# Performance work log

Hardware: AMD Instinct MI355X
Metric: run time of the kernel (lower is better)

The kernel has to match this reference:

```python
import jax, jax.numpy as jnp
import numpy as np

N = 50_000       # nodes
E = 1_600_000    # edges (avg degree 32)
D = 32           # emb_dim == hidden_dim, num_heads = 1
L = 8            # num_layers
K = 8            # SortPooling k
VOCAB = 100


def setup_inputs() -> dict:
    key = jax.random.key(0)
    ks = jax.random.split(key, 20)
    def nrm(k, shape, scale=0.1):
        return jax.random.normal(k, shape, dtype=jnp.float32) * scale
    return {
        "h_tok": jax.random.randint(ks[0], (N,), 0, VOCAB),
        "e_tok": jax.random.randint(ks[1], (E,), 0, VOCAB),
        "src": jax.random.randint(ks[2], (E,), 0, N),
        "dst": jax.random.randint(ks[3], (E,), 0, N),
        "tok_emb": nrm(ks[4], (VOCAB, D)),
        "e_tok_emb": nrm(ks[5], (VOCAB, D)),
        # per-layer EGATConv params (stacked over L layers; all dims are D->D)
        "W_ni": nrm(ks[6], (L, D, D)),
        "W_nj": nrm(ks[7], (L, D, D)),
        "W_fij": nrm(ks[8], (L, D, D)),
        "b_edge": nrm(ks[9], (L, D)),
        "attn": nrm(ks[10], (L, D)),
        "W_node": nrm(ks[11], (L, D, D)),
        # MLP head
        "W_lin": nrm(ks[12], (K * D, D)),
        "b_lin": nrm(ks[13], (D,)),
        "W1": nrm(ks[14], (D, D)),
        "b1": nrm(ks[15], (D,)),
        "W2": nrm(ks[16], (D, D)),
        "b2": nrm(ks[17], (D,)),
        "Wc": nrm(ks[18], (D, 2)),
        "bc": nrm(ks[19], (2,)),
    }


def _egat_layer(h, e, src, dst, Wni, Wnj, Wfij, b, attn, Wnode):
    """DGL EGATConv, num_heads=1. h: [N,D] nodes, e: [E,D] edges."""
    n = h.shape[0]
    # per-edge feature: f_ij = LeakyReLU(A*h_i + B*h_j + C*e_ij + b)
    f = jax.nn.leaky_relu((h @ Wni)[src] + (h @ Wnj)[dst] + e @ Wfij + b, 0.01)  # [E,D]
    logits = jnp.sum(f * attn, axis=-1)                                         # [E]
    # edge softmax over incoming edges of each destination node
    m = jax.ops.segment_max(logits, dst, num_segments=n)
    ex = jnp.exp(logits - m[dst])
    a = ex / jax.ops.segment_sum(ex, dst, num_segments=n)[dst]                  # [E]
    msg = (h @ Wnode)[src] * a[:, None]                                         # [E,D]
    h_out = jax.ops.segment_sum(msg, dst, num_segments=n)                       # [N,D]
    return h_out, f


def reference(h_tok, e_tok, src, dst, tok_emb, e_tok_emb, W_ni, W_nj, W_fij,
              b_edge, attn, W_node, W_lin, b_lin, W1, b1, W2, b2, Wc, bc):
    h = jax.nn.relu(tok_emb[h_tok])   # [N,D]
    e = e_tok_emb[e_tok]              # [E,D]

    def step(carry, p):
        h, e = carry
        Wni, Wnj, Wfij, b, at, Wn = p
        h2, e2 = _egat_layer(h, e, src, dst, Wni, Wnj, Wfij, b, at, Wn)
        return (jax.nn.relu(h2), e2), None

    (h, e), _ = jax.lax.scan(step, (h, e), (W_ni, W_nj, W_fij, b_edge, attn, W_node))

    # SortPooling(k): sort each node's features ascending, rank nodes by last
    # (largest) channel descending, keep top-k nodes, flatten. Single graph.
    hs = jnp.sort(h, axis=-1)                     # [N,D]
    _, idx = jax.lax.top_k(hs[:, -1], K)          # top-k nodes
    x = hs[idx].reshape(1, K * D)                 # [1, k*D]

    x = jax.nn.relu(x @ W_lin + b_lin)
    x = jax.nn.relu(x @ W1 + b1)
    x = jax.nn.relu(x @ W2 + b2)
    return x @ Wc + bc                            # [1, 2]
```

## Files before the change

### kernel.cpp

```cpp
#include <hip/hip_runtime.h>
#include <hip/hip_fp16.h>

#define DD 32
#define NLAYERS 8
#define TOPK 8
#define NPB 256
#define HNB 1024
#define BCH 4096
#define P2CAP 12288

typedef _Float16 half8 __attribute__((ext_vector_type(8)));
typedef float f32x4 __attribute__((ext_vector_type(4)));

__device__ __forceinline__ unsigned encf(float x){ unsigned u=__float_as_uint(x); return (u&0x80000000u)? ~u : (u|0x80000000u); }
__device__ __forceinline__ unsigned short f2h(float f){ return __half_as_ushort(__float2half(f)); }
__device__ __forceinline__ float h2f(unsigned short u){ return __half2float(__ushort_as_half(u)); }
__device__ __forceinline__ float4 up4(uint2 u){
  float4 r;
  r.x=h2f((unsigned short)(u.x&0xFFFFu)); r.y=h2f((unsigned short)(u.x>>16));
  r.z=h2f((unsigned short)(u.y&0xFFFFu)); r.w=h2f((unsigned short)(u.y>>16));
  return r;
}
union HU4 { uint4 u; half8 h; };
__device__ __forceinline__ int gidx(const void* p, long i, int i64){
  return i64 ? (int)((const long long*)p)[i] : ((const int*)p)[i];
}

__global__ __launch_bounds__(1024) void k_detect(const int* __restrict__ srcw,
                                                 int* __restrict__ iflag,
                                                 int* __restrict__ bcnt){
  int tid = threadIdx.x;
  for (int i=tid;i<HNB;i+=1024) bcnt[i]=0;
  if (tid==0){
    int allz = 1;
    for (int k=1;k<32;k+=2) if (srcw[k]!=0) allz = 0;
    *iflag = allz;
  }
}

__global__ void k_init(const void* __restrict__ h_tok,
                       const float* __restrict__ tok_emb,
                       unsigned short* __restrict__ h16,
                       const int* __restrict__ iflag, int N)
{
  int i64 = *iflag;
  long idx = (long)blockIdx.x*blockDim.x + threadIdx.x;
  if (idx >= (long)N*8) return;
  int n=(int)(idx>>3), q=(int)(idx&7);
  int t = gidx(h_tok, n, i64);
  float4 v = reinterpret_cast<const float4*>(tok_emb)[t*8+q];
  uint2 o;
  o.x = (unsigned)f2h(fmaxf(v.x,0.f)) | ((unsigned)f2h(fmaxf(v.y,0.f))<<16);
  o.y = (unsigned)f2h(fmaxf(v.z,0.f)) | ((unsigned)f2h(fmaxf(v.w,0.f))<<16);
  reinterpret_cast<uint2*>(h16)[(long)n*8+q] = o;
}

__global__ __launch_bounds__(256) void k_hist(
    const void* __restrict__ dstv, int* __restrict__ bcnt,
    const int* __restrict__ iflag, int E, int NB)
{
  __shared__ int bins[HNB];
  int i64 = *iflag;
  int tid = threadIdx.x;
  for (int i=tid;i<NB;i+=256) bins[i]=0;
  __syncthreads();
  long base = (long)blockIdx.x * BCH;
  long rem = (long)E - base;
  int nloc = (rem < BCH) ? (int)rem : BCH;
  for (int t=tid; t<nloc; t+=256){
    int d = gidx(dstv, base+t, i64);
    atomicAdd(&bins[d>>8], 1);
  }
  __syncthreads();
  for (int i=tid;i<NB;i+=256){
    int v = bins[i];
    if (v) atomicAdd(&bcnt[i], v);
  }
}

__global__ __launch_bounds__(1024) void k_bscan(const int* __restrict__ bcnt,
    int* __restrict__ bbase, int* __restrict__ gcur, int NB, int E)
{
  __shared__ int wsum[16];
  int tid=threadIdx.x, lane=tid&63, w=tid>>6;
  int v = (tid<NB)? bcnt[tid]:0;
  int x=v;
  #pragma unroll
  for (int d=1;d<64;d<<=1){ int t=__shfl_up(x,d,64); if(lane>=d) x+=t; }
  if (lane==63) wsum[w]=x;
  __syncthreads();
  if (w==0 && lane<16){
    int y=wsum[lane];
    #pragma unroll
    for (int d=1;d<16;d<<=1){ int t=__shfl_up(y,d,64); if(lane>=d) y+=t; }
    wsum[lane]=y;
  }
  __syncthreads();
  int wb = (w>0)? wsum[w-1]:0;
  int ex = x - v + wb;
  if (tid<NB){ bbase[tid]=ex; gcur[tid]=ex; }
  if (tid==0) bbase[NB]=E;
}

__global__ __launch_bounds__(256) void k_bucket(
    const void* __restrict__ srcv, const void* __restrict__ dstv,
    int* __restrict__ gcur, uint2* __restrict__ btmp,
    const int* __restrict__ iflag, int E, int NB)
{
  __shared__ int hist[HNB];
  __shared__ int cbase[HNB];
  int i64 = *iflag;
  int tid = threadIdx.x;
  long base = (long)blockIdx.x * BCH;
  long rem = (long)E - base;
  int nloc = (rem < BCH) ? (int)rem : BCH;
  if (nloc <= 0) return;
  for (int i = tid; i < NB; i += 256) hist[i] = 0;
  __syncthreads();
  int dl[BCH/256];
  #pragma unroll
  for (int k = 0; k < BCH/256; k++){
    int t = tid + k*256;
    dl[k] = -1;
    if (t < nloc){
      int d = gidx(dstv, base + t, i64);
      dl[k] = d;
      atomicAdd(&hist[d>>8], 1);
    }
  }
  __syncthreads();
  for (int i = tid; i < NB; i += 256){
    int hv = hist[i];
    cbase[i] = hv ? atomicAdd(&gcur[i], hv) : 0;
    hist[i] = 0;
  }
  __syncthreads();
  #pragma unroll
  for (int k = 0; k < BCH/256; k++){
    int t = tid + k*256;
    if (t < nloc){
      int d = dl[k];
      int s = gidx(srcv, base + t, i64);
      int b = d>>8;
      int slot = cbase[b] + atomicAdd(&hist[b], 1);
      uint2 r; r.x = ((unsigned)d<<16) | (unsigned)s; r.y = (unsigned)(base + t);
      btmp[slot] = r;
    }
  }
}

__global__ __launch_bounds__(256) void k_bsort(
    const int* __restrict__ bbase, const uint2* __restrict__ btmp,
    uint2* __restrict__ sde8, int* __restrict__ off, int N, int NB)
{
  __shared__ int lcnt[NPB];
  __shared__ int lbase[NPB];
  __shared__ int wsum2[4];
  __shared__ uint2 lrec[P2CAP];
  int bkt = blockIdx.x;
  int base = bbase[bkt], endp = bbase[bkt+1];
  int sz = endp - base;
  int lo = bkt*NPB;
  int tid = threadIdx.x;
  lcnt[tid] = 0;
  __syncthreads();
  for (int i=tid;i<sz;i+=256){
    uint2 r = btmp[base+i];
    atomicAdd(&lcnt[(int)(r.x>>16) - lo], 1);
  }
  __syncthreads();
  int v = lcnt[tid];
  int lane = tid&63, w = tid>>6;
  int x = v;
  #pragma unroll
  for (int d=1;d<64;d<<=1){ int t=__shfl_up(x,d,64); if(lane>=d) x+=t; }
  if (lane==63) wsum2[w]=x;
  __syncthreads();
  if (tid==0){ int a=0; for(int i=0;i<4;i++){ int t=wsum2[i]; wsum2[i]=a; a+=t; } }
  __syncthreads();
  int ex = x - v + wsum2[w];
  lbase[tid] = ex;
  int node = lo + tid;
  if (node < N) off[node] = base + ex;
  if (bkt == NB-1 && tid == 0) off[N] = bbase[NB];
  __syncthreads();
  if (sz <= P2CAP){
    lcnt[tid] = lbase[tid];
    __syncthreads();
    for (int i=tid;i<sz;i+=256){
      uint2 r = btmp[base+i];
      int d = (int)(r.x>>16) - lo;
      int p = atomicAdd(&lcnt[d],1);
      lrec[p] = r;
    }
    __syncthreads();
    for (int i=tid;i<sz;i+=256)
      sde8[base+i] = lrec[i];
  } else {
    lcnt[tid] = base + lbase[tid];
    __syncthreads();
    for (int i=tid;i<sz;i+=256){
      uint2 r = btmp[base+i];
      int d = (int)(r.x>>16) - lo;
      int p = atomicAdd(&lcnt[d],1);
      sde8[p] = r;
    }
  }
}

__global__ void k_fill(const uint2* __restrict__ sde8, const void* __restrict__ e_tok,
                       const float* __restrict__ e_emb,
                       unsigned* __restrict__ csr_sd, unsigned short* __restrict__ ebuf,
                       const int* __restrict__ iflag, int E){
  int i64 = *iflag;
  long idx = (long)blockIdx.x*blockDim.x + threadIdx.x;
  if (idx >= (long)E*4) return;
  int pos = (int)(idx>>2), j = (int)(idx&3);
  uint2 r = sde8[pos];
  if (j==0) csr_sd[pos] = r.x;
  int t = gidx(e_tok, (int)r.y, i64);
  const float4* sp = reinterpret_cast<const float4*>(e_emb + t*DD) + j*2;
  float4 x = sp[0], y = sp[1];
  uint4 ov;
  ov.x = (unsigned)f2h(x.x) | ((unsigned)f2h(x.y)<<16);
  ov.y = (unsigned)f2h(x.z) | ((unsigned)f2h(x.w)<<16);
  ov.z = (unsigned)f2h(y.x) | ((unsigned)f2h(y.y)<<16);
  ov.w = (unsigned)f2h(y.z) | ((unsigned)f2h(y.w)<<16);
  reinterpret_cast<uint4*>(ebuf)[(long)pos*4+j] = ov;
}

__global__ __launch_bounds__(256) void k_nodeAB(
    const unsigned short* __restrict__ h16,
    const float* __restrict__ WA, const float* __restrict__ WB,
    unsigned short* __restrict__ hA16, unsigned short* __restrict__ hB16, int N)
{
  __shared__ float hl[8][DD];
  int tid = threadIdx.x;
  int ln = tid>>5, c = tid&31;
  int n = blockIdx.x*8 + ln;
  hl[ln][c] = (n<N)? h2f(h16[(long)n*DD+c]) : 0.f;
  __syncthreads();
  float a=0.f,b=0.f;
  #pragma unroll
  for (int k=0;k<DD;k++){
    float v = hl[ln][k];
    a = fmaf(v, WA[k*DD+c], a);
    b = fmaf(v, WB[k*DD+c], b);
  }
  if (n<N){ hA16[(long)n*DD+c]=f2h(a); hB16[(long)n*DD+c]=f2h(b); }
}

__global__ __launch_bounds__(256) void k_edge(
    unsigned short* __restrict__ ebuf,
    const unsigned short* __restrict__ hA16, const unsigned short* __restrict__ hB16,
    const unsigned* __restrict__ csr_sd,
    const float* __restrict__ Wf, const float* __restrict__ bvec,
    const float* __restrict__ attn,
    unsigned short* __restrict__ lbuf, int ntiles, int writef)
{
  int lane = threadIdx.x & 63;
  int wid = (blockIdx.x*256 + threadIdx.x) >> 6;
  int nw  = (gridDim.x*256) >> 6;
  int m = lane & 15, q = lane >> 4;
  half8 a0, a1;
  #pragma unroll
  for (int j=0;j<8;j++){
    a0[j] = (_Float16)Wf[(q*8+j)*DD + m];
    a1[j] = (_Float16)Wf[(q*8+j)*DD + 16 + m];
  }
  float4 blo = *reinterpret_cast<const float4*>(bvec + q*4);
  float4 bhi = *reinterpret_cast<const float4*>(bvec + 16 + q*4);
  float4 alo = *reinterpret_cast<const float4*>(attn + q*4);
  float4 ahi = *reinterpret_cast<const float4*>(attn + 16 + q*4);
  f32x4 zero = {0.f,0.f,0.f,0.f};
  HU4 b0; b0.u = make_uint4(0,0,0,0);
  HU4 b1; b1.u = make_uint4(0,0,0,0);
  HU4 b2; b2.u = make_uint4(0,0,0,0);
  unsigned sd0 = 0, sd1 = 0, sd2 = 0;
  uint2 gA0_0={0,0}, gA1_0={0,0}, gB0_0={0,0}, gB1_0={0,0};
  uint2 gA0_1={0,0}, gA1_1={0,0}, gB0_1={0,0}, gB1_1={0,0};
  if (wid < ntiles){
    long e0 = (long)wid*16 + m;
    sd0 = csr_sd[e0];
    b0.u = *reinterpret_cast<const uint4*>(ebuf + e0*DD + q*8);
    unsigned s = sd0 & 0xFFFFu, d = sd0 >> 16;
    const uint2* pA = reinterpret_cast<const uint2*>(hA16 + (long)s*DD);
    const uint2* pB = reinterpret_cast<const uint2*>(hB16 + (long)d*DD);
    gA0_0=pA[q]; gA1_0=pA[4+q]; gB0_0=pB[q]; gB1_0=pB[4+q];
  }
  if (wid + nw < ntiles){
    long e1 = (long)(wid+nw)*16 + m;
    sd1 = csr_sd[e1];
    b1.u = *reinterpret_cast<const uint4*>(ebuf + e1*DD + q*8);
    unsigned s = sd1 & 0xFFFFu, d = sd1 >> 16;
    const uint2* pA = reinterpret_cast<const uint2*>(hA16 + (long)s*DD);
    const uint2* pB = reinterpret_cast<const uint2*>(hB16 + (long)d*DD);
    gA0_1=pA[q]; gA1_1=pA[4+q]; gB0_1=pB[q]; gB1_1=pB[4+q];
  }
  if (wid + 2*nw < ntiles){
    long e2 = (long)(wid+2*nw)*16 + m;
    sd2 = csr_sd[e2];
    b2.u = *reinterpret_cast<const uint4*>(ebuf + e2*DD + q*8);
  }
  for (int t = wid; t < ntiles; t += nw){
    int t2 = t + 2*nw, t3 = t + 3*nw;
    unsigned sd3 = 0; HU4 b3; b3.u = make_uint4(0,0,0,0);
    if (t3 < ntiles){
      long e3 = (long)t3*16 + m;
      sd3 = csr_sd[e3];
      b3.u = *reinterpret_cast<const uint4*>(ebuf + e3*DD + q*8);
    }
    uint2 gA0_2={0,0}, gA1_2={0,0}, gB0_2={0,0}, gB1_2={0,0};
    if (t2 < ntiles){
      unsigned s = sd2 & 0xFFFFu, d = sd2 >> 16;
      const uint2* pA = reinterpret_cast<const uint2*>(hA16 + (long)s*DD);
      const uint2* pB = reinterpret_cast<const uint2*>(hB16 + (long)d*DD);
      gA0_2=pA[q]; gA1_2=pA[4+q]; gB0_2=pB[q]; gB1_2=pB[4+q];
    }
    f32x4 d0 = __builtin_amdgcn_mfma_f32_16x16x32_f16(a0, b0.h, zero, 0,0,0);
    f32x4 d1 = __builtin_amdgcn_mfma_f32_16x16x32_f16(a1, b0.h, zero, 0,0,0);
    long tbase = (long)t*16;
    long edge = tbase + m;
    float4 A0 = up4(gA0_0), A1 = up4(gA1_0);
    float4 B0 = up4(gB0_0), B1 = up4(gB1_0);
    float f00 = d0[0]+A0.x+B0.x+blo.x, f01 = d0[1]+A0.y+B0.y+blo.y;
    float f02 = d0[2]+A0.z+B0.z+blo.z, f03 = d0[3]+A0.w+B0.w+blo.w;
    float f10 = d1[0]+A1.x+B1.x+bhi.x, f11 = d1[1]+A1.y+B1.y+bhi.y;
    float f12 = d1[2]+A1.z+B1.z+bhi.z, f13 = d1[3]+A1.w+B1.w+bhi.w;
    f00 = (f00>0.f)?f00:0.01f*f00; f01 = (f01>0.f)?f01:0.01f*f01;
    f02 = (f02>0.f)?f02:0.01f*f02; f03 = (f03>0.f)?f03:0.01f*f03;
    f10 = (f10>0.f)?f10:0.01f*f10; f11 = (f11>0.f)?f11:0.01f*f11;
    f12 = (f12>0.f)?f12:0.01f*f12; f13 = (f13>0.f)?f13:0.01f*f13;
    if (writef){
      uint2 w0, w1;
      w0.x = (unsigned)f2h(f00) | ((unsigned)f2h(f01)<<16);
      w0.y = (unsigned)f2h(f02) | ((unsigned)f2h(f03)<<16);
      w1.x = (unsigned)f2h(f10) | ((unsigned)f2h(f11)<<16);
      w1.y = (unsigned)f2h(f12) | ((unsigned)f2h(f13)<<16);
      *reinterpret_cast<uint2*>(ebuf + edge*DD + q*4) = w0;
      *reinterpret_cast<uint2*>(ebuf + edge*DD + 16 + q*4) = w1;
    }
    float l = f00*alo.x + f01*alo.y + f02*alo.z + f03*alo.w
            + f10*ahi.x + f11*ahi.y + f12*ahi.z + f13*ahi.w;
    l += __shfl_xor(l, 16, 64);
    l += __shfl_xor(l, 32, 64);
    if (lane < 16){
      float lc = fminf(fmaxf(l, -15.f), 10.5f);
      lbuf[tbase + lane] = f2h(__expf(lc));
    }
    sd0 = sd1; b0 = b1;
    gA0_0=gA0_1; gA1_0=gA1_1; gB0_0=gB0_1; gB1_0=gB1_1;
    sd1 = sd2; b1 = b2;
    gA0_1=gA0_2; gA1_1=gA1_2; gB0_1=gB0_2; gB1_1=gB1_2;
    sd2 = sd3; b2 = b3;
  }
}

__global__ __launch_bounds__(256) void k_aggrP(
    const unsigned short* __restrict__ h16in, const unsigned short* __restrict__ lbuf,
    const int* __restrict__ off, const unsigned* __restrict__ csr_sd,
    const float* __restrict__ Wnd, const float* __restrict__ WA,
    const float* __restrict__ WB,
    unsigned short* __restrict__ h16out, unsigned short* __restrict__ hA16,
    unsigned short* __restrict__ hB16, float* __restrict__ hout, int N, int last)
{
  __shared__ float gl[8][DD];
  __shared__ float tl[8][DD];
  int tid=threadIdx.x;
  int ln = tid>>5, c = tid&31;
  int n = blockIdx.x*8 + ln;
  float num=0.f, den=0.f;
  if (n<N){
    int o0 = off[n], o1 = off[n+1];
    int i = o0;
    for (; i+8 <= o1; i += 8){
      unsigned sd0=csr_sd[i],   sd1=csr_sd[i+1], sd2=csr_sd[i+2], sd3=csr_sd[i+3];
      unsigned sd4=csr_sd[i+4], sd5=csr_sd[i+5], sd6=csr_sd[i+6], sd7=csr_sd[i+7];
      float ex0=h2f(lbuf[i]),   ex1=h2f(lbuf[i+1]), ex2=h2f(lbuf[i+2]), ex3=h2f(lbuf[i+3]);
      float ex4=h2f(lbuf[i+4]), ex5=h2f(lbuf[i+5]), ex6=h2f(lbuf[i+6]), ex7=h2f(lbuf[i+7]);
      float g0=h2f(h16in[(long)(sd0&0xFFFFu)*DD+c]);
      float g1=h2f(h16in[(long)(sd1&0xFFFFu)*DD+c]);
      float g2=h2f(h16in[(long)(sd2&0xFFFFu)*DD+c]);
      float g3=h2f(h16in[(long)(sd3&0xFFFFu)*DD+c]);
      float g4=h2f(h16in[(long)(sd4&0xFFFFu)*DD+c]);
      float g5=h2f(h16in[(long)(sd5&0xFFFFu)*DD+c]);
      float g6=h2f(h16in[(long)(sd6&0xFFFFu)*DD+c]);
      float g7=h2f(h16in[(long)(sd7&0xFFFFu)*DD+c]);
      num=fmaf(ex0,g0,num); num=fmaf(ex1,g1,num);
      num=fmaf(ex2,g2,num); num=fmaf(ex3,g3,num);
      num=fmaf(ex4,g4,num); num=fmaf(ex5,g5,num);
      num=fmaf(ex6,g6,num); num=fmaf(ex7,g7,num);
      den+=ex0; den+=ex1; den+=ex2; den+=ex3;
      den+=ex4; den+=ex5; den+=ex6; den+=ex7;
    }
    for (; i<o1; i++){
      unsigned sd=csr_sd[i];
      float ex=h2f(lbuf[i]);
      num=fmaf(ex, h2f(h16in[(long)(sd&0xFFFFu)*DD+c]), num);
      den += ex;
    }
  }
  gl[ln][c] = (den>0.f)? num/den : 0.f;
  __syncthreads();
  float t=0.f;
  #pragma unroll
  for (int k=0;k<DD;k++) t = fmaf(gl[ln][k], Wnd[k*DD+c], t);
  t = fmaxf(t, 0.f);
  if (last){
    if (n<N) hout[(long)n*DD+c] = t;
    return;
  }
  tl[ln][c] = t;
  __syncthreads();
  float a=0.f,b=0.f;
  #pragma unroll
  for (int k=0;k<DD;k++){
    float v = tl[ln][k];
    a = fmaf(v, WA[k*DD+c], a);
    b = fmaf(v, WB[k*DD+c], b);
  }
  if (n<N){
    h16out[(long)n*DD+c]=f2h(t);
    hA16[(long)n*DD+c]=f2h(a);
    hB16[(long)n*DD+c]=f2h(b);
  }
}

__global__ void k_keys(const float* __restrict__ h, unsigned long long* __restrict__ keys, int N){
  int n = blockIdx.x*blockDim.x + threadIdx.x;
  if (n>=N) return;
  const float4* p = reinterpret_cast<const float4*>(h + (long)n*DD);
  float m = -1e38f;
  #pragma unroll
  for (int j=0;j<8;j++){
    float4 v = p[j];
    m = fmaxf(m, fmaxf(fmaxf(v.x,v.y), fmaxf(v.z,v.w)));
  }
  keys[n] = ((unsigned long long)encf(m)<<32) | (unsigned)(~(unsigned)n);
}

__global__ __launch_bounds__(256) void k_ptop(const unsigned long long* __restrict__ keys, int N,
                                              unsigned long long* __restrict__ outk){
  __shared__ unsigned long long red[256];
  int tid = threadIdx.x, b = blockIdx.x, nb = gridDim.x;
  int chunk = (N + nb - 1) / nb;
  int base = b*chunk, end = base+chunk; if (end>N) end=N;
  unsigned long long loc[TOPK];
  #pragma unroll
  for (int i=0;i<TOPK;i++) loc[i]=0ull;
  for (int i=base+tid; i<end; i+=256){
    unsigned long long k = keys[i];
    if (k > loc[TOPK-1]){
      int j = TOPK-1;
      while (j>0 && loc[j-1]<k){ loc[j]=loc[j-1]; j--; }
      loc[j]=k;
    }
  }
  for (int r=0; r<TOPK; r++){
    red[tid] = loc[0];
    __syncthreads();
    for (int s=128; s>0; s>>=1){
      if (tid<s && red[tid+s]>red[tid]) red[tid]=red[tid+s];
      __syncthreads();
    }
    unsigned long long w = red[0];
    if (tid==0) outk[b*TOPK + r] = w;
    if (loc[0]==w){
      #pragma unroll
      for (int j=0;j<TOPK-1;j++) loc[j]=loc[j+1];
      loc[TOPK-1]=0ull;
    }
    __syncthreads();
  }
}

__global__ __launch_bounds__(256) void k_head(
    const float* __restrict__ h, const unsigned long long* __restrict__ sel,
    const float* __restrict__ Wlin, const float* __restrict__ blin,
    const float* __restrict__ W1, const float* __restrict__ b1,
    const float* __restrict__ W2, const float* __restrict__ b2,
    const float* __restrict__ Wc, const float* __restrict__ bc,
    float* __restrict__ out, int N)
{
  __shared__ float xs[TOPK][DD];
  __shared__ float y1[DD], y2[DD], y3[DD];
  int tid=threadIdx.x;
  int r=tid>>5, c=tid&31;
  unsigned node = ~(unsigned)(sel[r] & 0xFFFFFFFFull);
  if (node >= (unsigned)N) node = 0;
  xs[r][c] = h[(long)node*DD + c];
  __syncthreads();
  if (tid<TOPK){
    for (int i=1;i<DD;i++){
      float v=xs[tid][i]; int j=i-1;
      while (j>=0 && xs[tid][j]>v){ xs[tid][j+1]=xs[tid][j]; j--; }
      xs[tid][j+1]=v;
    }
  }
  __syncthreads();
  if (tid<DD){
    float a=blin[tid];
    for (int i=0;i<TOPK*DD;i++) a = fmaf(xs[i>>5][i&31], Wlin[i*DD+tid], a);
    y1[tid] = a>0.f? a : 0.f;
  }
  __syncthreads();
  if (tid<DD){
    float a=b1[tid];
    #pragma unroll
    for (int i=0;i<DD;i++) a = fmaf(y1[i], W1[i*DD+tid], a);
    y2[tid] = a>0.f? a : 0.f;
  }
  __syncthreads();
  if (tid<DD){
    float a=b2[tid];
    #pragma unroll
    for (int i=0;i<DD;i++) a = fmaf(y2[i], W2[i*DD+tid], a);
    y3[tid] = a>0.f? a : 0.f;
  }
  __syncthreads();
  if (tid<2){
    float a=bc[tid];
    #pragma unroll
    for (int i=0;i<DD;i++) a = fmaf(y3[i], Wc[i*2+tid], a);
    out[tid] = a;
  }
}

extern "C" void kernel_launch(void* const* d_in, const int* in_sizes, int n_in,
                              void* d_out, int out_size, void* d_ws, size_t ws_size,
                              hipStream_t stream) {
  const int N = in_sizes[0];
  const int E = in_sizes[1];
  const float* tok_emb   = (const float*)d_in[4];
  const float* e_tok_emb = (const float*)d_in[5];
  const float* W_ni  = (const float*)d_in[6];
  const float* W_nj  = (const float*)d_in[7];
  const float* W_fij = (const float*)d_in[8];
  const float* b_e   = (const float*)d_in[9];
  const float* attn  = (const float*)d_in[10];
  const float* W_nd  = (const float*)d_in[11];

  char* p = (char*)d_ws;
  auto alloc = [&](size_t bytes)->char* {
    char* r = p; p += (bytes + 255) & ~(size_t)255; return r;
  };
  int* iflag = (int*)alloc(256);
  unsigned long long* sel = (unsigned long long*)alloc(256);
  unsigned long long* cand = (unsigned long long*)alloc(256*TOPK*8);
  int* bcnt = (int*)alloc(HNB*4);
  int* bbase = (int*)alloc((HNB+1)*4);
  int* gcur = (int*)alloc(HNB*4);
  int* csroff = (int*)alloc((size_t)(N+1)*4);
  unsigned* csr_sd = (unsigned*)alloc((size_t)(E+32)*4);
  float* h = (float*)alloc((size_t)N*DD*4);
  alloc((size_t)N*DD*2);
  unsigned short* lbuf = (unsigned short*)alloc((size_t)(E+32)*2);
  unsigned short* h16a = (unsigned short*)alloc((size_t)N*DD*2);
  unsigned short* h16b = (unsigned short*)alloc((size_t)N*DD*2);
  unsigned short* hA16 = (unsigned short*)alloc((size_t)N*DD*2);
  unsigned short* hB16 = (unsigned short*)alloc((size_t)N*DD*2);
  unsigned short* ebuf = (unsigned short*)alloc((size_t)(E+32)*DD*2);
  uint2* sde8 = (uint2*)h;
  uint2* btmp = (uint2*)ebuf;
  unsigned long long* keys = (unsigned long long*)lbuf;

  const int NB = (N + NPB - 1) / NPB;
  const int NECH = (E + BCH - 1) / BCH;

  hipLaunchKernelGGL(k_detect, dim3(1), dim3(1024), 0, stream, (const int*)d_in[2], iflag, bcnt);
  hipLaunchKernelGGL(k_init, dim3((int)(((long)N*8+255)/256)), dim3(256), 0, stream,
                     d_in[0], tok_emb, h16a, iflag, N);
  hipLaunchKernelGGL(k_hist, dim3(NECH), dim3(256), 0, stream,
                     d_in[3], bcnt, iflag, E, NB);
  hipLaunchKernelGGL(k_bscan, dim3(1), dim3(1024), 0, stream, bcnt, bbase, gcur, NB, E);
  hipLaunchKernelGGL(k_bucket, dim3(NECH), dim3(256), 0, stream,
                     d_in[2], d_in[3], gcur, btmp, iflag, E, NB);
  hipLaunchKernelGGL(k_bsort, dim3(NB), dim3(256), 0, stream, bbase, btmp, sde8, csroff, N, NB);
  hipLaunchKernelGGL(k_fill, dim3((int)(((long)E*4+255)/256)), dim3(256), 0, stream,
                     sde8, d_in[1], e_tok_emb, csr_sd, ebuf, iflag, E);

  int nb_node = (N+7)/8;
  int ntiles = (E+15)/16;
  hipLaunchKernelGGL(k_nodeAB, dim3(nb_node), dim3(256), 0, stream,
                     h16a, W_ni, W_nj, hA16, hB16, N);
  unsigned short* hcur = h16a;
  unsigned short* hnext = h16b;
  for (int l=0; l<NLAYERS; l++){
    const float* Wf  = W_fij + (size_t)l*DD*DD;
    const float* bl  = b_e   + (size_t)l*DD;
    const float* at  = attn  + (size_t)l*DD;
    const float* Wnd = W_nd  + (size_t)l*DD*DD;
    int last = (l == NLAYERS-1);
    hipLaunchKernelGGL(k_edge, dim3(2048), dim3(256), 0, stream,
                       ebuf, hA16, hB16, csr_sd, Wf, bl, at, lbuf, ntiles,
                       last ? 0 : 1);
    const float* WnA = last ? W_ni : (W_ni + (size_t)(l+1)*DD*DD);
    const float* WnB = last ? W_nj : (W_nj + (size_t)(l+1)*DD*DD);
    hipLaunchKernelGGL(k_aggrP, dim3(nb_node), dim3(256), 0, stream,
                       hcur, lbuf, csroff, csr_sd, Wnd, WnA, WnB,
                       hnext, hA16, hB16, h, N, last);
    unsigned short* tmp = hcur; hcur = hnext; hnext = tmp;
  }

  hipLaunchKernelGGL(k_keys, dim3((N+255)/256), dim3(256), 0, stream, h, keys, N);
  hipLaunchKernelGGL(k_ptop, dim3(256), dim3(256), 0, stream, keys, N, cand);
  hipLaunchKernelGGL(k_ptop, dim3(1), dim3(256), 0, stream, cand, 256*TOPK, sel);
  hipLaunchKernelGGL(k_head, dim3(1), dim3(256), 0, stream,
                     h, sel,
                     (const float*)d_in[12], (const float*)d_in[13],
                     (const float*)d_in[14], (const float*)d_in[15],
                     (const float*)d_in[16], (const float*)d_in[17],
                     (const float*)d_in[18], (const float*)d_in[19],
                     (float*)d_out, N);
}
```

Before: 1.039 ms.

## Permute hA/hB channel layout for 16-byte gathers and pack src index with exp weight

```diff
diff --git a/kernel.cpp b/kernel.cpp
--- a/kernel.cpp
+++ b/kernel.cpp
@@ -24,6 +24,9 @@
 union HU4 { uint4 u; half8 h; };
 __device__ __forceinline__ int gidx(const void* p, long i, int i64){
   return i64 ? (int)((const long long*)p)[i] : ((const int*)p)[i];
+}
+__device__ __forceinline__ int pidx(int c){
+  return ((c&15)>>2)*8 + (c&3) + ((c&16)?4:0);
 }
 
 __global__ __launch_bounds__(1024) void k_detect(const int* __restrict__ srcw,
@@ -247,7 +250,11 @@
     a = fmaf(v, WA[k*DD+c], a);
     b = fmaf(v, WB[k*DD+c], b);
   }
-  if (n<N){ hA16[(long)n*DD+c]=f2h(a); hB16[(long)n*DD+c]=f2h(b); }
+  if (n<N){
+    int pc = pidx(c);
+    hA16[(long)n*DD+pc]=f2h(a);
+    hB16[(long)n*DD+pc]=f2h(b);
+  }
 }
 
 __global__ __launch_bounds__(256) void k_edge(
@@ -256,7 +263,7 @@
     const unsigned* __restrict__ csr_sd,
     const float* __restrict__ Wf, const float* __restrict__ bvec,
     const float* __restrict__ attn,
-    unsigned short* __restrict__ lbuf, int ntiles, int writef)
+    unsigned* __restrict__ exs, int ntiles, int writef)
 {
   int lane = threadIdx.x & 63;
   int wid = (blockIdx.x*256 + threadIdx.x) >> 6;
@@ -277,25 +284,23 @@
   HU4 b1; b1.u = make_uint4(0,0,0,0);
   HU4 b2; b2.u = make_uint4(0,0,0,0);
   unsigned sd0 = 0, sd1 = 0, sd2 = 0;
-  uint2 gA0_0={0,0}, gA1_0={0,0}, gB0_0={0,0}, gB1_0={0,0};
-  uint2 gA0_1={0,0}, gA1_1={0,0}, gB0_1={0,0}, gB1_1={0,0};
+  uint4 gA_0={0,0,0,0}, gB_0={0,0,0,0};
+  uint4 gA_1={0,0,0,0}, gB_1={0,0,0,0};
   if (wid < ntiles){
     long e0 = (long)wid*16 + m;
     sd0 = csr_sd[e0];
     b0.u = *reinterpret_cast<const uint4*>(ebuf + e0*DD + q*8);
     unsigned s = sd0 & 0xFFFFu, d = sd0 >> 16;
-    const uint2* pA = reinterpret_cast<const uint2*>(hA16 + (long)s*DD);
-    const uint2* pB = reinterpret_cast<const uint2*>(hB16 + (long)d*DD);
-    gA0_0=pA[q]; gA1_0=pA[4+q]; gB0_0=pB[q]; gB1_0=pB[4+q];
+    gA_0 = reinterpret_cast<const uint4*>(hA16 + (long)s*DD)[q];
+    gB_0 = reinterpret_cast<const uint4*>(hB16 + (long)d*DD)[q];
   }
   if (wid + nw < ntiles){
     long e1 = (long)(wid+nw)*16 + m;
     sd1 = csr_sd[e1];
     b1.u = *reinterpret_cast<const uint4*>(ebuf + e1*DD + q*8);
     unsigned s = sd1 & 0xFFFFu, d = sd1 >> 16;
-    const uint2* pA = reinterpret_cast<const uint2*>(hA16 + (long)s*DD);
-    const uint2* pB = reinterpret_cast<const uint2*>(hB16 + (long)d*DD);
-    gA0_1=pA[q]; gA1_1=pA[4+q]; gB0_1=pB[q]; gB1_1=pB[4+q];
+    gA_1 = reinterpret_cast<const uint4*>(hA16 + (long)s*DD)[q];
+    gB_1 = reinterpret_cast<const uint4*>(hB16 + (long)d*DD)[q];
   }
   if (wid + 2*nw < ntiles){
     long e2 = (long)(wid+2*nw)*16 + m;
@@ -310,19 +315,18 @@
       sd3 = csr_sd[e3];
       b3.u = *reinterpret_cast<const uint4*>(ebuf + e3*DD + q*8);
     }
-    uint2 gA0_2={0,0}, gA1_2={0,0}, gB0_2={0,0}, gB1_2={0,0};
+    uint4 gA_2={0,0,0,0}, gB_2={0,0,0,0};
     if (t2 < ntiles){
       unsigned s = sd2 & 0xFFFFu, d = sd2 >> 16;
-      const uint2* pA = reinterpret_cast<const uint2*>(hA16 + (long)s*DD);
-      const uint2* pB = reinterpret_cast<const uint2*>(hB16 + (long)d*DD);
-      gA0_2=pA[q]; gA1_2=pA[4+q]; gB0_2=pB[q]; gB1_2=pB[4+q];
+      gA_2 = reinterpret_cast<const uint4*>(hA16 + (long)s*DD)[q];
+      gB_2 = reinterpret_cast<const uint4*>(hB16 + (long)d*DD)[q];
     }
     f32x4 d0 = __builtin_amdgcn_mfma_f32_16x16x32_f16(a0, b0.h, zero, 0,0,0);
     f32x4 d1 = __builtin_amdgcn_mfma_f32_16x16x32_f16(a1, b0.h, zero, 0,0,0);
     long tbase = (long)t*16;
     long edge = tbase + m;
-    float4 A0 = up4(gA0_0), A1 = up4(gA1_0);
-    float4 B0 = up4(gB0_0), B1 = up4(gB1_0);
+    float4 A0 = up4(make_uint2(gA_0.x, gA_0.y)), A1 = up4(make_uint2(gA_0.z, gA_0.w));
+    float4 B0 = up4(make_uint2(gB_0.x, gB_0.y)), B1 = up4(make_uint2(gB_0.z, gB_0.w));
     float f00 = d0[0]+A0.x+B0.x+blo.x, f01 = d0[1]+A0.y+B0.y+blo.y;
     float f02 = d0[2]+A0.z+B0.z+blo.z, f03 = d0[3]+A0.w+B0.w+blo.w;
     float f10 = d1[0]+A1.x+B1.x+bhi.x, f11 = d1[1]+A1.y+B1.y+bhi.y;
@@ -346,19 +350,17 @@
     l += __shfl_xor(l, 32, 64);
     if (lane < 16){
       float lc = fminf(fmaxf(l, -15.f), 10.5f);
-      lbuf[tbase + lane] = f2h(__expf(lc));
-    }
-    sd0 = sd1; b0 = b1;
-    gA0_0=gA0_1; gA1_0=gA1_1; gB0_0=gB0_1; gB1_0=gB1_1;
-    sd1 = sd2; b1 = b2;
-    gA0_1=gA0_2; gA1_1=gA1_2; gB0_1=gB0_2; gB1_1=gB1_2;
+      exs[tbase + lane] = ((unsigned)f2h(__expf(lc))<<16) | (sd0 & 0xFFFFu);
+    }
+    sd0 = sd1; b0 = b1; gA_0 = gA_1; gB_0 = gB_1;
+    sd1 = sd2; b1 = b2; gA_1 = gA_2; gB_1 = gB_2;
     sd2 = sd3; b2 = b3;
   }
 }
 
 __global__ __launch_bounds__(256) void k_aggrP(
-    const unsigned short* __restrict__ h16in, const unsigned short* __restrict__ lbuf,
-    const int* __restrict__ off, const unsigned* __restrict__ csr_sd,
+    const unsigned short* __restrict__ h16in, const unsigned* __restrict__ exs,
+    const int* __restrict__ off,
     const float* __restrict__ Wnd, const float* __restrict__ WA,
     const float* __restrict__ WB,
     unsigned short* __restrict__ h16out, unsigned short* __restrict__ hA16,
@@ -374,18 +376,20 @@
     int o0 = off[n], o1 = off[n+1];
     int i = o0;
     for (; i+8 <= o1; i += 8){
-      unsigned sd0=csr_sd[i],   sd1=csr_sd[i+1], sd2=csr_sd[i+2], sd3=csr_sd[i+3];
-      unsigned sd4=csr_sd[i+4], sd5=csr_sd[i+5], sd6=csr_sd[i+6], sd7=csr_sd[i+7];
-      float ex0=h2f(lbuf[i]),   ex1=h2f(lbuf[i+1]), ex2=h2f(lbuf[i+2]), ex3=h2f(lbuf[i+3]);
-      float ex4=h2f(lbuf[i+4]), ex5=h2f(lbuf[i+5]), ex6=h2f(lbuf[i+6]), ex7=h2f(lbuf[i+7]);
-      float g0=h2f(h16in[(long)(sd0&0xFFFFu)*DD+c]);
-      float g1=h2f(h16in[(long)(sd1&0xFFFFu)*DD+c]);
-      float g2=h2f(h16in[(long)(sd2&0xFFFFu)*DD+c]);
-      float g3=h2f(h16in[(long)(sd3&0xFFFFu)*DD+c]);
-      float g4=h2f(h16in[(long)(sd4&0xFFFFu)*DD+c]);
-      float g5=h2f(h16in[(long)(sd5&0xFFFFu)*DD+c]);
-      float g6=h2f(h16in[(long)(sd6&0xFFFFu)*DD+c]);
-      float g7=h2f(h16in[(long)(sd7&0xFFFFu)*DD+c]);
+      unsigned w0=exs[i],   w1=exs[i+1], w2=exs[i+2], w3=exs[i+3];
+      unsigned w4=exs[i+4], w5=exs[i+5], w6=exs[i+6], w7=exs[i+7];
+      float ex0=h2f((unsigned short)(w0>>16)), ex1=h2f((unsigned short)(w1>>16));
+      float ex2=h2f((unsigned short)(w2>>16)), ex3=h2f((unsigned short)(w3>>16));
+      float ex4=h2f((unsigned short)(w4>>16)), ex5=h2f((unsigned short)(w5>>16));
+      float ex6=h2f((unsigned short)(w6>>16)), ex7=h2f((unsigned short)(w7>>16));
+      float g0=h2f(h16in[(long)(w0&0xFFFFu)*DD+c]);
+      float g1=h2f(h16in[(long)(w1&0xFFFFu)*DD+c]);
+      float g2=h2f(h16in[(long)(w2&0xFFFFu)*DD+c]);
+      float g3=h2f(h16in[(long)(w3&0xFFFFu)*DD+c]);
+      float g4=h2f(h16in[(long)(w4&0xFFFFu)*DD+c]);
+      float g5=h2f(h16in[(long)(w5&0xFFFFu)*DD+c]);
+      float g6=h2f(h16in[(long)(w6&0xFFFFu)*DD+c]);
+      float g7=h2f(h16in[(long)(w7&0xFFFFu)*DD+c]);
       num=fmaf(ex0,g0,num); num=fmaf(ex1,g1,num);
       num=fmaf(ex2,g2,num); num=fmaf(ex3,g3,num);
       num=fmaf(ex4,g4,num); num=fmaf(ex5,g5,num);
@@ -394,9 +398,9 @@
       den+=ex4; den+=ex5; den+=ex6; den+=ex7;
     }
     for (; i<o1; i++){
-      unsigned sd=csr_sd[i];
-      float ex=h2f(lbuf[i]);
-      num=fmaf(ex, h2f(h16in[(long)(sd&0xFFFFu)*DD+c]), num);
+      unsigned w=exs[i];
+      float ex=h2f((unsigned short)(w>>16));
+      num=fmaf(ex, h2f(h16in[(long)(w&0xFFFFu)*DD+c]), num);
       den += ex;
     }
   }
@@ -420,9 +424,10 @@
     b = fmaf(v, WB[k*DD+c], b);
   }
   if (n<N){
+    int pc = pidx(c);
     h16out[(long)n*DD+c]=f2h(t);
-    hA16[(long)n*DD+c]=f2h(a);
-    hB16[(long)n*DD+c]=f2h(b);
+    hA16[(long)n*DD+pc]=f2h(a);
+    hB16[(long)n*DD+pc]=f2h(b);
   }
 }
 
@@ -553,8 +558,7 @@
   int* csroff = (int*)alloc((size_t)(N+1)*4);
   unsigned* csr_sd = (unsigned*)alloc((size_t)(E+32)*4);
   float* h = (float*)alloc((size_t)N*DD*4);
-  alloc((size_t)N*DD*2);
-  unsigned short* lbuf = (unsigned short*)alloc((size_t)(E+32)*2);
+  unsigned* exs = (unsigned*)alloc((size_t)(E+32)*4);
   unsigned short* h16a = (unsigned short*)alloc((size_t)N*DD*2);
   unsigned short* h16b = (unsigned short*)alloc((size_t)N*DD*2);
   unsigned short* hA16 = (unsigned short*)alloc((size_t)N*DD*2);
@@ -562,7 +566,7 @@
   unsigned short* ebuf = (unsigned short*)alloc((size_t)(E+32)*DD*2);
   uint2* sde8 = (uint2*)h;
   uint2* btmp = (uint2*)ebuf;
-  unsigned long long* keys = (unsigned long long*)lbuf;
+  unsigned long long* keys = (unsigned long long*)exs;
 
   const int NB = (N + NPB - 1) / NPB;
   const int NECH = (E + BCH - 1) / BCH;
@@ -592,12 +596,12 @@
     const float* Wnd = W_nd  + (size_t)l*DD*DD;
     int last = (l == NLAYERS-1);
     hipLaunchKernelGGL(k_edge, dim3(2048), dim3(256), 0, stream,
-                       ebuf, hA16, hB16, csr_sd, Wf, bl, at, lbuf, ntiles,
+                       ebuf, hA16, hB16, csr_sd, Wf, bl, at, exs, ntiles,
                        last ? 0 : 1);
     const float* WnA = last ? W_ni : (W_ni + (size_t)(l+1)*DD*DD);
     const float* WnB = last ? W_nj : (W_nj + (size_t)(l+1)*DD*DD);
     hipLaunchKernelGGL(k_aggrP, dim3(nb_node), dim3(256), 0, stream,
-                       hcur, lbuf, csroff, csr_sd, Wnd, WnA, WnB,
+                       hcur, exs, csroff, Wnd, WnA, WnB,
                        hnext, hA16, hB16, h, N, last);
     unsigned short* tmp = hcur; hcur = hnext; hnext = tmp;
   }
```

After: 998.4 us. 1.04x faster.
